# Kernel optimization log

Measured on AMD Instinct MI355X. Metric: run time of the kernel, lower is better.

The kernel has to match this reference:

```python
import jax, jax.numpy as jnp
from jax import lax
import numpy as np

NUM_LAYERS = 4
NUM_HEADS = 4
FUTURE_FRAMES = 2
EPS = 1e-5  # torch default for BatchNorm1d and LayerNorm


def setup_inputs() -> dict:
    key = jax.random.key(0)
    ks = jax.random.split(key, 8)
    B, F, T, C2, BC = 1024, 257, 3, 3, 32
    IN_DIM = T * C2 * 2  # 18
    L, H = NUM_LAYERS, NUM_HEADS
    s = 0.1
    inp = {
        "x": jax.random.normal(ks[0], (B, F, T, C2, 2), dtype=jnp.float32),
        "in_w": jax.random.normal(ks[1], (IN_DIM, BC), dtype=jnp.float32) * s,
        "in_b": jnp.zeros((BC,), jnp.float32),
        "conv_w": jax.random.normal(ks[2], (L, 3, BC, BC), dtype=jnp.float32) * s,  # (L, W, Cin, Cout)
        "bn_g": jnp.ones((L, BC), jnp.float32),
        "bn_b": jnp.zeros((L, BC), jnp.float32),
        "qkv_w": jax.random.normal(ks[3], (L, BC, 3 * BC), dtype=jnp.float32) * s,
        "proj_w": jax.random.normal(ks[4], (L, BC, BC), dtype=jnp.float32) * s,
        "proj_b": jnp.zeros((L, BC), jnp.float32),
        "ln_g": jnp.ones((L, BC), jnp.float32),
        "ln_b": jnp.zeros((L, BC), jnp.float32),
        "h1_w": jax.random.normal(ks[5], (BC, BC // 2), dtype=jnp.float32) * s,
        "h1_b": jnp.zeros((BC // 2,), jnp.float32),
        "h2_w": jax.random.normal(ks[6], (BC // 2, 1), dtype=jnp.float32) * s,
        "h2_b": jnp.zeros((1,), jnp.float32),
    }
    return inp


def _banded_attention(x, qkv_w, proj_w, proj_b):
    # x: (B, F, C); window = [i, i + FUTURE_FRAMES]
    B, F, C = x.shape
    H, D = NUM_HEADS, C // NUM_HEADS
    qkv = x @ qkv_w                                   # (B, F, 3C)
    q, k, v = jnp.split(qkv, 3, axis=-1)
    q = q.reshape(B, F, H, D)
    k = k.reshape(B, F, H, D)
    v = v.reshape(B, F, H, D)
    scores = jnp.einsum("bihd,bjhd->bhij", q, k) * (D ** -0.5)
    i = jnp.arange(F)[:, None]
    j = jnp.arange(F)[None, :]
    allowed = (j >= i) & (j <= i + FUTURE_FRAMES)     # width-3 band
    scores = jnp.where(allowed, scores, -jnp.inf)
    attn = jax.nn.softmax(scores, axis=-1)
    out = jnp.einsum("bhij,bjhd->bihd", attn, v).reshape(B, F, C)
    return out @ proj_w + proj_b


def _layer(x, cw, bg, bb, qw, pw, pb, lg, lb):
    # conv over freq axis, channels-last: (B, F, C)
    c = lax.conv_general_dilated(x, cw, window_strides=(1,), padding="SAME",
                                 dimension_numbers=("NWC", "WIO", "NWC"))
    # BatchNorm1d in training mode: stats over (batch, freq), biased variance
    mu = c.mean(axis=(0, 1))
    var = c.var(axis=(0, 1))
    c = (c - mu) * lax.rsqrt(var + EPS) * bg + bb
    c = jax.nn.gelu(c, approximate=False)             # nn.GELU exact
    y = c + _banded_attention(x, qw, pw, pb)
    m = y.mean(axis=-1, keepdims=True)
    v = y.var(axis=-1, keepdims=True)
    return (y - m) * lax.rsqrt(v + EPS) * lg + lb


def reference(x, in_w, in_b, conv_w, bn_g, bn_b, qkv_w, proj_w, proj_b,
              ln_g, ln_b, h1_w, h1_b, h2_w, h2_b):
    B, F = x.shape[0], x.shape[1]
    h = x.reshape(B, F, -1) @ in_w + in_b             # (B, F, 32)
    for l in range(NUM_LAYERS):
        h = _layer(h, conv_w[l], bn_g[l], bn_b[l], qkv_w[l],
                   proj_w[l], proj_b[l], ln_g[l], ln_b[l])
    s = jax.nn.gelu(h @ h1_w + h1_b, approximate=False)
    mask = jax.nn.sigmoid(s @ h2_w + h2_b)            # (B, F, 1)
    return mask
```

## Files before the change

### kernel.cpp

```cpp
#include <hip/hip_runtime.h>
#include <math.h>


#define BB 1024
#define FF 257
#define BF (BB*FF)
#define TILE 64
#define NT 5
#define NBLK (BB*NT)
#define NLAYER 4
#define SQ 36

__device__ __forceinline__ float gelu_exact(float x){
    return 0.5f*x*(1.0f+erff(x*0.70710678118654752f));
}
__device__ __forceinline__ float dot4(float4 a, float4 b, float acc){
    return fmaf(a.x,b.x,fmaf(a.y,b.y,fmaf(a.z,b.z,fmaf(a.w,b.w,acc))));
}

__global__ __launch_bounds__(256) void k_zero(float* __restrict__ stats){
    stats[threadIdx.x]=0.0f;
}

__global__ __launch_bounds__(256) void k_inproj(const float* __restrict__ x,
        const float* __restrict__ in_w, const float* __restrict__ in_b,
        float* __restrict__ h)
{
    __shared__ float xs[TILE*18];
    int b = blockIdx.x / NT, t = blockIdx.x % NT, t0 = t*TILE;
    int tid = threadIdx.x;
    int nv = min(TILE, FF-t0);
    for (int i=tid;i<nv*18;i+=256) xs[i]=x[(size_t)(b*FF+t0)*18+i];
    __syncthreads();
    int co=tid&31, rq=tid>>5, rbase=rq*8;
    float bias = in_b[co];
    float a0=bias,a1=bias,a2=bias,a3=bias,a4=bias,a5=bias,a6=bias,a7=bias;
    #pragma unroll
    for (int ci=0;ci<18;ci++){
        float w = in_w[ci*32+co];
        a0=fmaf(xs[(rbase+0)*18+ci],w,a0);
        a1=fmaf(xs[(rbase+1)*18+ci],w,a1);
        a2=fmaf(xs[(rbase+2)*18+ci],w,a2);
        a3=fmaf(xs[(rbase+3)*18+ci],w,a3);
        a4=fmaf(xs[(rbase+4)*18+ci],w,a4);
        a5=fmaf(xs[(rbase+5)*18+ci],w,a5);
        a6=fmaf(xs[(rbase+6)*18+ci],w,a6);
        a7=fmaf(xs[(rbase+7)*18+ci],w,a7);
    }
    size_t base=(size_t)(b*FF+t0+rbase)*32+co;
    if (rbase+0<nv) h[base+0*32]=a0;
    if (rbase+1<nv) h[base+1*32]=a1;
    if (rbase+2<nv) h[base+2*32]=a2;
    if (rbase+3<nv) h[base+3*32]=a3;
    if (rbase+4<nv) h[base+4*32]=a4;
    if (rbase+5<nv) h[base+5*32]=a5;
    if (rbase+6<nv) h[base+6*32]=a6;
    if (rbase+7<nv) h[base+7*32]=a7;
}

#define CONV_C4_BODY(HSROW) \
    { float4 hv; \
      hv=*(const float4*)(HSROW+0*32); a0=dot4(hv,w0,a0); \
      hv=*(const float4*)(HSROW+1*32); a0=dot4(hv,w1,a0); a1=dot4(hv,w0,a1); \
      hv=*(const float4*)(HSROW+2*32); a0=dot4(hv,w2,a0); a1=dot4(hv,w1,a1); a2=dot4(hv,w0,a2); \
      hv=*(const float4*)(HSROW+3*32); a1=dot4(hv,w2,a1); a2=dot4(hv,w1,a2); a3=dot4(hv,w0,a3); \
      hv=*(const float4*)(HSROW+4*32); a2=dot4(hv,w2,a2); a3=dot4(hv,w1,a3); a4=dot4(hv,w0,a4); \
      hv=*(const float4*)(HSROW+5*32); a3=dot4(hv,w2,a3); a4=dot4(hv,w1,a4); a5=dot4(hv,w0,a5); \
      hv=*(const float4*)(HSROW+6*32); a4=dot4(hv,w2,a4); a5=dot4(hv,w1,a5); a6=dot4(hv,w0,a6); \
      hv=*(const float4*)(HSROW+7*32); a5=dot4(hv,w2,a5); a6=dot4(hv,w1,a6); a7=dot4(hv,w0,a7); \
      hv=*(const float4*)(HSROW+8*32); a6=dot4(hv,w2,a6); a7=dot4(hv,w1,a7); \
      hv=*(const float4*)(HSROW+9*32); a7=dot4(hv,w2,a7); }

__global__ __launch_bounds__(256) void k_convstats(const float* __restrict__ h,
        const float* __restrict__ conv_w, int layer, float* __restrict__ partials)
{
    __shared__ float hs[66*32];
    __shared__ float ps[8][32];
    __shared__ float pq[8][32];
    int b=blockIdx.x/NT, t=blockIdx.x%NT, t0=t*TILE, tid=threadIdx.x;
    for (int i4=tid;i4<66*8;i4+=256){
        int r=i4>>3, f=t0-1+r;
        float4 v=make_float4(0.f,0.f,0.f,0.f);
        if (f>=0 && f<FF) v=*(const float4*)(h+(size_t)(b*FF+f)*32+(i4&7)*4);
        *(float4*)&hs[r*32+(i4&7)*4]=v;
    }
    __syncthreads();
    int co=tid&31, rq=tid>>5, rbase=rq*8;
    const float* wl = conv_w + layer*3072 + co;
    float a0=0.f,a1=0.f,a2=0.f,a3=0.f,a4=0.f,a5=0.f,a6=0.f,a7=0.f;
    #pragma unroll 1
    for (int c4=0;c4<8;c4++){
        const float* w=wl+c4*128;
        float4 w0=make_float4(w[0],   w[32],  w[64],  w[96]);
        float4 w1=make_float4(w[1024],w[1056],w[1088],w[1120]);
        float4 w2=make_float4(w[2048],w[2080],w[2112],w[2144]);
        const float* hb=&hs[rbase*32+c4*4];
        CONV_C4_BODY(hb)
    }
    float ssum=0.f, ssq=0.f;
    if (t0+rbase+0<FF){ ssum+=a0; ssq+=a0*a0; }
    if (t0+rbase+1<FF){ ssum+=a1; ssq+=a1*a1; }
    if (t0+rbase+2<FF){ ssum+=a2; ssq+=a2*a2; }
    if (t0+rbase+3<FF){ ssum+=a3; ssq+=a3*a3; }
    if (t0+rbase+4<FF){ ssum+=a4; ssq+=a4*a4; }
    if (t0+rbase+5<FF){ ssum+=a5; ssq+=a5*a5; }
    if (t0+rbase+6<FF){ ssum+=a6; ssq+=a6*a6; }
    if (t0+rbase+7<FF){ ssum+=a7; ssq+=a7*a7; }
    ps[rq][co]=ssum; pq[rq][co]=ssq;
    __syncthreads();
    if (tid<32){
        float s=0.f;
        #pragma unroll
        for(int q=0;q<8;q++) s+=ps[q][tid];
        partials[blockIdx.x*64+tid]=s;
    } else if (tid<64){
        int cc=tid-32;
        float s=0.f;
        #pragma unroll
        for(int q=0;q<8;q++) s+=pq[q][cc];
        partials[blockIdx.x*64+tid]=s;
    }
}

__global__ __launch_bounds__(256) void k_reduce(const float* __restrict__ partials,
        float* __restrict__ stats)
{
    __shared__ float sm[4][64];
    int tid=threadIdx.x, col=tid&63, rq=tid>>6;
    int r0=blockIdx.x*80;
    float s=0.f;
    for (int k=rq;k<80;k+=4) s += partials[(r0+k)*64+col];
    sm[rq][col]=s;
    __syncthreads();
    if (tid<64){
        float v=sm[0][tid]+sm[1][tid]+sm[2][tid]+sm[3][tid];
        atomicAdd(&stats[tid], v);
    }
}

#define LN_STORE(Y,K) { \
    float s=(Y); \
    s+=__shfl_xor(s,1); s+=__shfl_xor(s,2); s+=__shfl_xor(s,4); \
    s+=__shfl_xor(s,8); s+=__shfl_xor(s,16); \
    float m=s*(1.0f/32.0f); \
    float dd=(Y)-m; float v=dd*dd; \
    v+=__shfl_xor(v,1); v+=__shfl_xor(v,2); v+=__shfl_xor(v,4); \
    v+=__shfl_xor(v,8); v+=__shfl_xor(v,16); \
    float rsd=rsqrtf(v*(1.0f/32.0f)+1e-5f); \
    if (t0+rbase+(K)<FF) hn[(size_t)(b*FF+t0+rbase+(K))*32+co]=dd*rsd*lgv+lbv; }

__global__ __launch_bounds__(256) void k_layer(const float* __restrict__ h,
        float* __restrict__ hn, const float* __restrict__ stats,
        const float* __restrict__ conv_w, const float* __restrict__ bn_g,
        const float* __restrict__ bn_b, const float* __restrict__ qkv_w,
        const float* __restrict__ proj_w, const float* __restrict__ proj_b,
        const float* __restrict__ ln_g, const float* __restrict__ ln_b, int layer)
{
    __shared__ float hs[67*32];
    __shared__ float qs[66*SQ];
    __shared__ float ks[66*SQ];
    __shared__ float vs[66*SQ];

    int b=blockIdx.x/NT, t=blockIdx.x%NT, t0=t*TILE, tid=threadIdx.x;
    for (int i4=tid;i4<67*8;i4+=256){
        int r=i4>>3, f=t0-1+r;
        float4 v=make_float4(0.f,0.f,0.f,0.f);
        if (f>=0 && f<FF) v=*(const float4*)(h+(size_t)(b*FF+f)*32+(i4&7)*4);
        *(float4*)&hs[r*32+(i4&7)*4]=v;
    }
    __syncthreads();

    int co=tid&31, rq=tid>>5, rbase=rq*8;
    float y0,y1,y2,y3,y4,y5,y6,y7;
    {
        float mu  = stats[co]*(1.0f/(float)BF);
        float var = stats[32+co]*(1.0f/(float)BF) - mu*mu;
        float rs  = rsqrtf(fmaxf(var,0.f)+1e-5f);
        float g   = bn_g[layer*32+co];
        float scv = g*rs;
        float shv = bn_b[layer*32+co] - mu*g*rs;
        const float* wcl = conv_w + layer*3072 + co;
        const float* wql = qkv_w + layer*3072 + co;
        float a0=0.f,a1=0.f,a2=0.f,a3=0.f,a4=0.f,a5=0.f,a6=0.f,a7=0.f;
        float q0=0.f,q1=0.f,q2=0.f,q3=0.f,q4=0.f,q5=0.f,q6=0.f,q7=0.f;
        float k0=0.f,k1=0.f,k2=0.f,k3=0.f,k4=0.f,k5=0.f,k6=0.f,k7=0.f;
        float v0=0.f,v1=0.f,v2=0.f,v3=0.f,v4=0.f,v5=0.f,v6=0.f,v7=0.f;
        float ek=0.f, ev=0.f;
        int edge = (tid<64);
        #pragma unroll 1
        for (int c4=0;c4<8;c4++){
            const float* w=wcl+c4*128;
            float4 w0=make_float4(w[0],   w[32],  w[64],  w[96]);
            float4 w1=make_float4(w[1024],w[1056],w[1088],w[1120]);
            float4 w2=make_float4(w[2048],w[2080],w[2112],w[2144]);
            const float* qw=wql+c4*384;
            float4 wq=make_float4(qw[0],  qw[96], qw[192],qw[288]);
            float4 wk=make_float4(qw[32], qw[128],qw[224],qw[320]);
            float4 wv=make_float4(qw[64], qw[160],qw[256],qw[352]);
            const float* hb=&hs[rbase*32+c4*4];
            float4 hv;
            hv=*(const float4*)(hb+0*32); a0=dot4(hv,w0,a0);
            hv=*(const float4*)(hb+1*32); a0=dot4(hv,w1,a0); a1=dot4(hv,w0,a1);
                q0=dot4(hv,wq,q0); k0=dot4(hv,wk,k0); v0=dot4(hv,wv,v0);
            hv=*(const float4*)(hb+2*32); a0=dot4(hv,w2,a0); a1=dot4(hv,w1,a1); a2=dot4(hv,w0,a2);
                q1=dot4(hv,wq,q1); k1=dot4(hv,wk,k1); v1=dot4(hv,wv,v1);
            hv=*(const float4*)(hb+3*32); a1=dot4(hv,w2,a1); a2=dot4(hv,w1,a2); a3=dot4(hv,w0,a3);
                q2=dot4(hv,wq,q2); k2=dot4(hv,wk,k2); v2=dot4(hv,wv,v2);
            hv=*(const float4*)(hb+4*32); a2=dot4(hv,w2,a2); a3=dot4(hv,w1,a3); a4=dot4(hv,w0,a4);
                q3=dot4(hv,wq,q3); k3=dot4(hv,wk,k3); v3=dot4(hv,wv,v3);
            hv=*(const float4*)(hb+5*32); a3=dot4(hv,w2,a3); a4=dot4(hv,w1,a4); a5=dot4(hv,w0,a5);
                q4=dot4(hv,wq,q4); k4=dot4(hv,wk,k4); v4=dot4(hv,wv,v4);
            hv=*(const float4*)(hb+6*32); a4=dot4(hv,w2,a4); a5=dot4(hv,w1,a5); a6=dot4(hv,w0,a6);
                q5=dot4(hv,wq,q5); k5=dot4(hv,wk,k5); v5=dot4(hv,wv,v5);
            hv=*(const float4*)(hb+7*32); a5=dot4(hv,w2,a5); a6=dot4(hv,w1,a6); a7=dot4(hv,w0,a7);
                q6=dot4(hv,wq,q6); k6=dot4(hv,wk,k6); v6=dot4(hv,wv,v6);
            hv=*(const float4*)(hb+8*32); a6=dot4(hv,w2,a6); a7=dot4(hv,w1,a7);
                q7=dot4(hv,wq,q7); k7=dot4(hv,wk,k7); v7=dot4(hv,wv,v7);
            hv=*(const float4*)(hb+9*32); a7=dot4(hv,w2,a7);
            if (edge){
                float4 he=*(const float4*)(&hs[(65+rq)*32+c4*4]);
                ek=dot4(he,wk,ek); ev=dot4(he,wv,ev);
            }
        }
        y0=gelu_exact(fmaf(a0,scv,shv));
        y1=gelu_exact(fmaf(a1,scv,shv));
        y2=gelu_exact(fmaf(a2,scv,shv));
        y3=gelu_exact(fmaf(a3,scv,shv));
        y4=gelu_exact(fmaf(a4,scv,shv));
        y5=gelu_exact(fmaf(a5,scv,shv));
        y6=gelu_exact(fmaf(a6,scv,shv));
        y7=gelu_exact(fmaf(a7,scv,shv));
        int rb=rbase*SQ+co;
        qs[rb+0*SQ]=q0; ks[rb+0*SQ]=k0; vs[rb+0*SQ]=v0;
        qs[rb+1*SQ]=q1; ks[rb+1*SQ]=k1; vs[rb+1*SQ]=v1;
        qs[rb+2*SQ]=q2; ks[rb+2*SQ]=k2; vs[rb+2*SQ]=v2;
        qs[rb+3*SQ]=q3; ks[rb+3*SQ]=k3; vs[rb+3*SQ]=v3;
        qs[rb+4*SQ]=q4; ks[rb+4*SQ]=k4; vs[rb+4*SQ]=v4;
        qs[rb+5*SQ]=q5; ks[rb+5*SQ]=k5; vs[rb+5*SQ]=v5;
        qs[rb+6*SQ]=q6; ks[rb+6*SQ]=k6; vs[rb+6*SQ]=v6;
        qs[rb+7*SQ]=q7; ks[rb+7*SQ]=k7; vs[rb+7*SQ]=v7;
        if (edge){ ks[(64+rq)*SQ+co]=ek; vs[(64+rq)*SQ+co]=ev; }
    }
    __syncthreads();

    {
        int r=tid>>2, hh=tid&3, f=t0+r;
        if (f<FF){
            int base=hh*8;
            float4 qa=*(const float4*)&qs[r*SQ+base];
            float4 qb=*(const float4*)&qs[r*SQ+base+4];
            float s0, s1=-1e30f, s2=-1e30f;
            s0=dot4(qa,*(const float4*)&ks[r*SQ+base],
               dot4(qb,*(const float4*)&ks[r*SQ+base+4],0.f))*0.35355339059327373f;
            if (f+1<FF)
                s1=dot4(qa,*(const float4*)&ks[(r+1)*SQ+base],
                   dot4(qb,*(const float4*)&ks[(r+1)*SQ+base+4],0.f))*0.35355339059327373f;
            if (f+2<FF)
                s2=dot4(qa,*(const float4*)&ks[(r+2)*SQ+base],
                   dot4(qb,*(const float4*)&ks[(r+2)*SQ+base+4],0.f))*0.35355339059327373f;
            float mx=fmaxf(s0,fmaxf(s1,s2));
            float e0=expf(s0-mx);
            float e1=(f+1<FF)?expf(s1-mx):0.f;
            float e2=(f+2<FF)?expf(s2-mx):0.f;
            float inv=1.0f/(e0+e1+e2);
            float4 va=*(const float4*)&vs[r*SQ+base];
            float4 vb=*(const float4*)&vs[r*SQ+base+4];
            float4 oa=make_float4(e0*va.x,e0*va.y,e0*va.z,e0*va.w);
            float4 ob=make_float4(e0*vb.x,e0*vb.y,e0*vb.z,e0*vb.w);
            if (f+1<FF){
                va=*(const float4*)&vs[(r+1)*SQ+base];
                vb=*(const float4*)&vs[(r+1)*SQ+base+4];
                oa.x=fmaf(e1,va.x,oa.x); oa.y=fmaf(e1,va.y,oa.y);
                oa.z=fmaf(e1,va.z,oa.z); oa.w=fmaf(e1,va.w,oa.w);
                ob.x=fmaf(e1,vb.x,ob.x); ob.y=fmaf(e1,vb.y,ob.y);
                ob.z=fmaf(e1,vb.z,ob.z); ob.w=fmaf(e1,vb.w,ob.w);
            }
            if (f+2<FF){
                va=*(const float4*)&vs[(r+2)*SQ+base];
                vb=*(const float4*)&vs[(r+2)*SQ+base+4];
                oa.x=fmaf(e2,va.x,oa.x); oa.y=fmaf(e2,va.y,oa.y);
                oa.z=fmaf(e2,va.z,oa.z); oa.w=fmaf(e2,va.w,oa.w);
                ob.x=fmaf(e2,vb.x,ob.x); ob.y=fmaf(e2,vb.y,ob.y);
                ob.z=fmaf(e2,vb.z,ob.z); ob.w=fmaf(e2,vb.w,ob.w);
            }
            oa.x*=inv; oa.y*=inv; oa.z*=inv; oa.w*=inv;
            ob.x*=inv; ob.y*=inv; ob.z*=inv; ob.w*=inv;
            *(float4*)&qs[r*SQ+base]=oa;
            *(float4*)&qs[r*SQ+base+4]=ob;
        }
    }
    __syncthreads();

    {
        const float* pwl = proj_w + layer*1024 + co;
        float pbv = proj_b[layer*32+co];
        float d0=pbv,d1=pbv,d2=pbv,d3=pbv,d4=pbv,d5=pbv,d6=pbv,d7=pbv;
        #pragma unroll 1
        for (int c4=0;c4<8;c4++){
            const float* w=pwl+c4*128;
            float4 wv=make_float4(w[0],w[32],w[64],w[96]);
            const float* qb=&qs[rbase*SQ+c4*4];
            d0=dot4(*(const float4*)(qb+0*SQ),wv,d0);
            d1=dot4(*(const float4*)(qb+1*SQ),wv,d1);
            d2=dot4(*(const float4*)(qb+2*SQ),wv,d2);
            d3=dot4(*(const float4*)(qb+3*SQ),wv,d3);
            d4=dot4(*(const float4*)(qb+4*SQ),wv,d4);
            d5=dot4(*(const float4*)(qb+5*SQ),wv,d5);
            d6=dot4(*(const float4*)(qb+6*SQ),wv,d6);
            d7=dot4(*(const float4*)(qb+7*SQ),wv,d7);
        }
        y0+=d0; y1+=d1; y2+=d2; y3+=d3; y4+=d4; y5+=d5; y6+=d6; y7+=d7;
    }

    {
        float lgv=ln_g[layer*32+co];
        float lbv=ln_b[layer*32+co];
        LN_STORE(y0,0) LN_STORE(y1,1) LN_STORE(y2,2) LN_STORE(y3,3)
        LN_STORE(y4,4) LN_STORE(y5,5) LN_STORE(y6,6) LN_STORE(y7,7)
    }
}

__global__ __launch_bounds__(256) void k_head(const float* __restrict__ h,
        const float* __restrict__ h1_w, const float* __restrict__ h1_b,
        const float* __restrict__ h2_w, const float* __restrict__ h2_b,
        float* __restrict__ out)
{
    __shared__ float hs[256*SQ];
    __shared__ float w1t[16*32];
    int tid=threadIdx.x;
    int r0=blockIdx.x*256;
    for (int i4=tid;i4<256*8;i4+=256){
        float4 v=*(const float4*)(h+(size_t)r0*32+i4*4);
        *(float4*)&hs[(i4>>3)*SQ+(i4&7)*4]=v;
    }
    for (int i=tid;i<512;i+=256) w1t[i]=h1_w[(i&31)*16+(i>>5)];
    __syncthreads();
    float4 hv0=*(const float4*)&hs[tid*SQ+ 0];
    float4 hv1=*(const float4*)&hs[tid*SQ+ 4];
    float4 hv2=*(const float4*)&hs[tid*SQ+ 8];
    float4 hv3=*(const float4*)&hs[tid*SQ+12];
    float4 hv4=*(const float4*)&hs[tid*SQ+16];
    float4 hv5=*(const float4*)&hs[tid*SQ+20];
    float4 hv6=*(const float4*)&hs[tid*SQ+24];
    float4 hv7=*(const float4*)&hs[tid*SQ+28];
    float acc2=h2_b[0];
    #pragma unroll
    for (int j=0;j<16;j++){
        const float* wr=&w1t[j*32];
        float aj=h1_b[j];
        aj=dot4(hv0,*(const float4*)(wr+ 0),aj);
        aj=dot4(hv1,*(const float4*)(wr+ 4),aj);
        aj=dot4(hv2,*(const float4*)(wr+ 8),aj);
        aj=dot4(hv3,*(const float4*)(wr+12),aj);
        aj=dot4(hv4,*(const float4*)(wr+16),aj);
        aj=dot4(hv5,*(const float4*)(wr+20),aj);
        aj=dot4(hv6,*(const float4*)(wr+24),aj);
        aj=dot4(hv7,*(const float4*)(wr+28),aj);
        acc2=fmaf(gelu_exact(aj), h2_w[j], acc2);
    }
    out[r0+tid]=1.0f/(1.0f+expf(-acc2));
}

extern "C" void kernel_launch(void* const* d_in, const int* in_sizes, int n_in,
                              void* d_out, int out_size, void* d_ws, size_t ws_size,
                              hipStream_t stream)
{
    const float* x     =(const float*)d_in[0];
    const float* in_w  =(const float*)d_in[1];
    const float* in_b  =(const float*)d_in[2];
    const float* conv_w=(const float*)d_in[3];
    const float* bn_g  =(const float*)d_in[4];
    const float* bn_b  =(const float*)d_in[5];
    const float* qkv_w =(const float*)d_in[6];
    const float* proj_w=(const float*)d_in[7];
    const float* proj_b=(const float*)d_in[8];
    const float* ln_g  =(const float*)d_in[9];
    const float* ln_b  =(const float*)d_in[10];
    const float* h1_w  =(const float*)d_in[11];
    const float* h1_b  =(const float*)d_in[12];
    const float* h2_w  =(const float*)d_in[13];
    const float* h2_b  =(const float*)d_in[14];

    float* bufA     = (float*)d_ws;
    float* bufB     = bufA + (size_t)BF*32;
    float* partials = bufB + (size_t)BF*32;
    float* stats    = partials + (size_t)NBLK*64;

    k_zero<<<1,256,0,stream>>>(stats);
    k_inproj<<<NBLK,256,0,stream>>>(x,in_w,in_b,bufA);
    for (int l=0;l<NLAYER;l++){
        float* cur = (l&1)? bufB : bufA;
        float* nxt = (l&1)? bufA : bufB;
        k_convstats<<<NBLK,256,0,stream>>>(cur, conv_w, l, partials);
        k_reduce<<<64,256,0,stream>>>(partials, stats + l*64);
        k_layer<<<NBLK,256,0,stream>>>(cur, nxt, stats+l*64, conv_w, bn_g, bn_b,
                                       qkv_w, proj_w, proj_b, ln_g, ln_b, l);
    }
    k_head<<<1028,256,0,stream>>>(bufA, h1_w,h1_b,h2_w,h2_b, (float*)d_out);
}
```

Baseline: 712.6 us.

## Store conv output in stats pass and reuse it in layer kernel

The conv+stats kernel now writes the raw convolution output to the next-layer buffer. The layer kernel reads those values back instead of recomputing the 3-tap convolution, and its shared halo shrinks by one row. This removes duplicated conv FMAs and weight loads in the layer kernel, at the cost of an extra full-tensor global write and read per layer. Separately, expf is replaced by the fast __expf intrinsic in the softmax and the sigmoid. The same buffer is passed as both the __restrict__ input and the output of the layer kernel, which only stays correct because each thread reads its own elements before writing them.

```diff
diff --git a/kernel.cpp b/kernel.cpp
--- a/kernel.cpp
+++ b/kernel.cpp
@@ -71,8 +71,9 @@
       hv=*(const float4*)(HSROW+8*32); a6=dot4(hv,w2,a6); a7=dot4(hv,w1,a7); \
       hv=*(const float4*)(HSROW+9*32); a7=dot4(hv,w2,a7); }
 
-__global__ __launch_bounds__(256) void k_convstats(const float* __restrict__ h,
-        const float* __restrict__ conv_w, int layer, float* __restrict__ partials)
+__global__ __launch_bounds__(256) void k_conv(const float* __restrict__ h,
+        const float* __restrict__ conv_w, int layer, float* __restrict__ c,
+        float* __restrict__ partials)
 {
     __shared__ float hs[66*32];
     __shared__ float ps[8][32];
@@ -97,15 +98,16 @@
         const float* hb=&hs[rbase*32+c4*4];
         CONV_C4_BODY(hb)
     }
+    size_t base=(size_t)(b*FF+t0+rbase)*32+co;
     float ssum=0.f, ssq=0.f;
-    if (t0+rbase+0<FF){ ssum+=a0; ssq+=a0*a0; }
-    if (t0+rbase+1<FF){ ssum+=a1; ssq+=a1*a1; }
-    if (t0+rbase+2<FF){ ssum+=a2; ssq+=a2*a2; }
-    if (t0+rbase+3<FF){ ssum+=a3; ssq+=a3*a3; }
-    if (t0+rbase+4<FF){ ssum+=a4; ssq+=a4*a4; }
-    if (t0+rbase+5<FF){ ssum+=a5; ssq+=a5*a5; }
-    if (t0+rbase+6<FF){ ssum+=a6; ssq+=a6*a6; }
-    if (t0+rbase+7<FF){ ssum+=a7; ssq+=a7*a7; }
+    if (t0+rbase+0<FF){ ssum+=a0; ssq+=a0*a0; c[base+0*32]=a0; }
+    if (t0+rbase+1<FF){ ssum+=a1; ssq+=a1*a1; c[base+1*32]=a1; }
+    if (t0+rbase+2<FF){ ssum+=a2; ssq+=a2*a2; c[base+2*32]=a2; }
+    if (t0+rbase+3<FF){ ssum+=a3; ssq+=a3*a3; c[base+3*32]=a3; }
+    if (t0+rbase+4<FF){ ssum+=a4; ssq+=a4*a4; c[base+4*32]=a4; }
+    if (t0+rbase+5<FF){ ssum+=a5; ssq+=a5*a5; c[base+5*32]=a5; }
+    if (t0+rbase+6<FF){ ssum+=a6; ssq+=a6*a6; c[base+6*32]=a6; }
+    if (t0+rbase+7<FF){ ssum+=a7; ssq+=a7*a7; c[base+7*32]=a7; }
     ps[rq][co]=ssum; pq[rq][co]=ssq;
     __syncthreads();
     if (tid<32){
@@ -150,22 +152,23 @@
     if (t0+rbase+(K)<FF) hn[(size_t)(b*FF+t0+rbase+(K))*32+co]=dd*rsd*lgv+lbv; }
 
 __global__ __launch_bounds__(256) void k_layer(const float* __restrict__ h,
-        float* __restrict__ hn, const float* __restrict__ stats,
-        const float* __restrict__ conv_w, const float* __restrict__ bn_g,
-        const float* __restrict__ bn_b, const float* __restrict__ qkv_w,
-        const float* __restrict__ proj_w, const float* __restrict__ proj_b,
-        const float* __restrict__ ln_g, const float* __restrict__ ln_b, int layer)
-{
-    __shared__ float hs[67*32];
+        float* __restrict__ hn, const float* __restrict__ cv,
+        const float* __restrict__ stats,
+        const float* __restrict__ bn_g, const float* __restrict__ bn_b,
+        const float* __restrict__ qkv_w, const float* __restrict__ proj_w,
+        const float* __restrict__ proj_b, const float* __restrict__ ln_g,
+        const float* __restrict__ ln_b, int layer)
+{
+    __shared__ float hs[66*32];
     __shared__ float qs[66*SQ];
     __shared__ float ks[66*SQ];
     __shared__ float vs[66*SQ];
 
     int b=blockIdx.x/NT, t=blockIdx.x%NT, t0=t*TILE, tid=threadIdx.x;
-    for (int i4=tid;i4<67*8;i4+=256){
-        int r=i4>>3, f=t0-1+r;
+    for (int i4=tid;i4<66*8;i4+=256){
+        int r=i4>>3, f=t0+r;
         float4 v=make_float4(0.f,0.f,0.f,0.f);
-        if (f>=0 && f<FF) v=*(const float4*)(h+(size_t)(b*FF+f)*32+(i4&7)*4);
+        if (f<FF) v=*(const float4*)(h+(size_t)(b*FF+f)*32+(i4&7)*4);
         *(float4*)&hs[r*32+(i4&7)*4]=v;
     }
     __syncthreads();
@@ -179,9 +182,26 @@
         float g   = bn_g[layer*32+co];
         float scv = g*rs;
         float shv = bn_b[layer*32+co] - mu*g*rs;
-        const float* wcl = conv_w + layer*3072 + co;
+        size_t base=(size_t)(b*FF+t0+rbase)*32+co;
+        float c0=(t0+rbase+0<FF)?cv[base+0*32]:0.f;
+        float c1=(t0+rbase+1<FF)?cv[base+1*32]:0.f;
+        float c2=(t0+rbase+2<FF)?cv[base+2*32]:0.f;
+        float c3=(t0+rbase+3<FF)?cv[base+3*32]:0.f;
+        float c4v=(t0+rbase+4<FF)?cv[base+4*32]:0.f;
+        float c5=(t0+rbase+5<FF)?cv[base+5*32]:0.f;
+        float c6=(t0+rbase+6<FF)?cv[base+6*32]:0.f;
+        float c7=(t0+rbase+7<FF)?cv[base+7*32]:0.f;
+        y0=gelu_exact(fmaf(c0,scv,shv));
+        y1=gelu_exact(fmaf(c1,scv,shv));
+        y2=gelu_exact(fmaf(c2,scv,shv));
+        y3=gelu_exact(fmaf(c3,scv,shv));
+        y4=gelu_exact(fmaf(c4v,scv,shv));
+        y5=gelu_exact(fmaf(c5,scv,shv));
+        y6=gelu_exact(fmaf(c6,scv,shv));
+        y7=gelu_exact(fmaf(c7,scv,shv));
+    }
+    {
         const float* wql = qkv_w + layer*3072 + co;
-        float a0=0.f,a1=0.f,a2=0.f,a3=0.f,a4=0.f,a5=0.f,a6=0.f,a7=0.f;
         float q0=0.f,q1=0.f,q2=0.f,q3=0.f,q4=0.f,q5=0.f,q6=0.f,q7=0.f;
         float k0=0.f,k1=0.f,k2=0.f,k3=0.f,k4=0.f,k5=0.f,k6=0.f,k7=0.f;
         float v0=0.f,v1=0.f,v2=0.f,v3=0.f,v4=0.f,v5=0.f,v6=0.f,v7=0.f;
@@ -189,47 +209,25 @@
         int edge = (tid<64);
         #pragma unroll 1
         for (int c4=0;c4<8;c4++){
-            const float* w=wcl+c4*128;
-            float4 w0=make_float4(w[0],   w[32],  w[64],  w[96]);
-            float4 w1=make_float4(w[1024],w[1056],w[1088],w[1120]);
-            float4 w2=make_float4(w[2048],w[2080],w[2112],w[2144]);
             const float* qw=wql+c4*384;
             float4 wq=make_float4(qw[0],  qw[96], qw[192],qw[288]);
             float4 wk=make_float4(qw[32], qw[128],qw[224],qw[320]);
             float4 wv=make_float4(qw[64], qw[160],qw[256],qw[352]);
             const float* hb=&hs[rbase*32+c4*4];
             float4 hv;
-            hv=*(const float4*)(hb+0*32); a0=dot4(hv,w0,a0);
-            hv=*(const float4*)(hb+1*32); a0=dot4(hv,w1,a0); a1=dot4(hv,w0,a1);
-                q0=dot4(hv,wq,q0); k0=dot4(hv,wk,k0); v0=dot4(hv,wv,v0);
-            hv=*(const float4*)(hb+2*32); a0=dot4(hv,w2,a0); a1=dot4(hv,w1,a1); a2=dot4(hv,w0,a2);
-                q1=dot4(hv,wq,q1); k1=dot4(hv,wk,k1); v1=dot4(hv,wv,v1);
-            hv=*(const float4*)(hb+3*32); a1=dot4(hv,w2,a1); a2=dot4(hv,w1,a2); a3=dot4(hv,w0,a3);
-                q2=dot4(hv,wq,q2); k2=dot4(hv,wk,k2); v2=dot4(hv,wv,v2);
-            hv=*(const float4*)(hb+4*32); a2=dot4(hv,w2,a2); a3=dot4(hv,w1,a3); a4=dot4(hv,w0,a4);
-                q3=dot4(hv,wq,q3); k3=dot4(hv,wk,k3); v3=dot4(hv,wv,v3);
-            hv=*(const float4*)(hb+5*32); a3=dot4(hv,w2,a3); a4=dot4(hv,w1,a4); a5=dot4(hv,w0,a5);
-                q4=dot4(hv,wq,q4); k4=dot4(hv,wk,k4); v4=dot4(hv,wv,v4);
-            hv=*(const float4*)(hb+6*32); a4=dot4(hv,w2,a4); a5=dot4(hv,w1,a5); a6=dot4(hv,w0,a6);
-                q5=dot4(hv,wq,q5); k5=dot4(hv,wk,k5); v5=dot4(hv,wv,v5);
-            hv=*(const float4*)(hb+7*32); a5=dot4(hv,w2,a5); a6=dot4(hv,w1,a6); a7=dot4(hv,w0,a7);
-                q6=dot4(hv,wq,q6); k6=dot4(hv,wk,k6); v6=dot4(hv,wv,v6);
-            hv=*(const float4*)(hb+8*32); a6=dot4(hv,w2,a6); a7=dot4(hv,w1,a7);
-                q7=dot4(hv,wq,q7); k7=dot4(hv,wk,k7); v7=dot4(hv,wv,v7);
-            hv=*(const float4*)(hb+9*32); a7=dot4(hv,w2,a7);
+            hv=*(const float4*)(hb+0*32); q0=dot4(hv,wq,q0); k0=dot4(hv,wk,k0); v0=dot4(hv,wv,v0);
+            hv=*(const float4*)(hb+1*32); q1=dot4(hv,wq,q1); k1=dot4(hv,wk,k1); v1=dot4(hv,wv,v1);
+            hv=*(const float4*)(hb+2*32); q2=dot4(hv,wq,q2); k2=dot4(hv,wk,k2); v2=dot4(hv,wv,v2);
+            hv=*(const float4*)(hb+3*32); q3=dot4(hv,wq,q3); k3=dot4(hv,wk,k3); v3=dot4(hv,wv,v3);
+            hv=*(const float4*)(hb+4*32); q4=dot4(hv,wq,q4); k4=dot4(hv,wk,k4); v4=dot4(hv,wv,v4);
+            hv=*(const float4*)(hb+5*32); q5=dot4(hv,wq,q5); k5=dot4(hv,wk,k5); v5=dot4(hv,wv,v5);
+            hv=*(const float4*)(hb+6*32); q6=dot4(hv,wq,q6); k6=dot4(hv,wk,k6); v6=dot4(hv,wv,v6);
+            hv=*(const float4*)(hb+7*32); q7=dot4(hv,wq,q7); k7=dot4(hv,wk,k7); v7=dot4(hv,wv,v7);
             if (edge){
-                float4 he=*(const float4*)(&hs[(65+rq)*32+c4*4]);
+                float4 he=*(const float4*)(&hs[(64+rq)*32+c4*4]);
                 ek=dot4(he,wk,ek); ev=dot4(he,wv,ev);
             }
         }
-        y0=gelu_exact(fmaf(a0,scv,shv));
-        y1=gelu_exact(fmaf(a1,scv,shv));
-        y2=gelu_exact(fmaf(a2,scv,shv));
-        y3=gelu_exact(fmaf(a3,scv,shv));
-        y4=gelu_exact(fmaf(a4,scv,shv));
-        y5=gelu_exact(fmaf(a5,scv,shv));
-        y6=gelu_exact(fmaf(a6,scv,shv));
-        y7=gelu_exact(fmaf(a7,scv,shv));
         int rb=rbase*SQ+co;
         qs[rb+0*SQ]=q0; ks[rb+0*SQ]=k0; vs[rb+0*SQ]=v0;
         qs[rb+1*SQ]=q1; ks[rb+1*SQ]=k1; vs[rb+1*SQ]=v1;
@@ -259,9 +257,9 @@
                 s2=dot4(qa,*(const float4*)&ks[(r+2)*SQ+base],
                    dot4(qb,*(const float4*)&ks[(r+2)*SQ+base+4],0.f))*0.35355339059327373f;
             float mx=fmaxf(s0,fmaxf(s1,s2));
-            float e0=expf(s0-mx);
-            float e1=(f+1<FF)?expf(s1-mx):0.f;
-            float e2=(f+2<FF)?expf(s2-mx):0.f;
+            float e0=__expf(s0-mx);
+            float e1=(f+1<FF)?__expf(s1-mx):0.f;
+            float e2=(f+2<FF)?__expf(s2-mx):0.f;
             float inv=1.0f/(e0+e1+e2);
             float4 va=*(const float4*)&vs[r*SQ+base];
             float4 vb=*(const float4*)&vs[r*SQ+base+4];
@@ -358,7 +356,7 @@
         aj=dot4(hv7,*(const float4*)(wr+28),aj);
         acc2=fmaf(gelu_exact(aj), h2_w[j], acc2);
     }
-    out[r0+tid]=1.0f/(1.0f+expf(-acc2));
+    out[r0+tid]=1.0f/(1.0f+__expf(-acc2));
 }
 
 extern "C" void kernel_launch(void* const* d_in, const int* in_sizes, int n_in,
@@ -391,9 +389,9 @@
     for (int l=0;l<NLAYER;l++){
         float* cur = (l&1)? bufB : bufA;
         float* nxt = (l&1)? bufA : bufB;
-        k_convstats<<<NBLK,256,0,stream>>>(cur, conv_w, l, partials);
+        k_conv<<<NBLK,256,0,stream>>>(cur, conv_w, l, nxt, partials);
         k_reduce<<<64,256,0,stream>>>(partials, stats + l*64);
-        k_layer<<<NBLK,256,0,stream>>>(cur, nxt, stats+l*64, conv_w, bn_g, bn_b,
+        k_layer<<<NBLK,256,0,stream>>>(cur, nxt, nxt, stats+l*64, bn_g, bn_b,
                                        qkv_w, proj_w, proj_b, ln_g, ln_b, l);
     }
     k_head<<<1028,256,0,stream>>>(bufA, h1_w,h1_b,h2_w,h2_b, (float*)d_out);
```

New measurement: 599.9 us. 15.8% less time.
